# Performance work log

Hardware: AMD Instinct MI355X
Metric: run time of the kernel (lower is better)

The kernel has to match this reference:

```python
import jax, jax.numpy as jnp
import numpy as np
from jax.scipy.special import logsumexp

EPS = 0.1
MAX_ITER = 100
STAB = 1e-6
N_CLASS = 100
BATCH = 4096


def setup_inputs() -> dict:
    key = jax.random.key(0)
    k1, k2 = jax.random.split(key)
    pred = jax.random.normal(k1, (BATCH, N_CLASS), dtype=jnp.float32)
    target = jax.random.randint(k2, (BATCH,), 0, N_CLASS, dtype=jnp.int64)
    return {"pred": pred, "target": target}


def _cost_matrix_euclidean(n_class):
    c = jnp.arange(n_class, dtype=jnp.float32)
    C = (c[None, :] - c[:, None]) ** 2  # [n, n]
    cmax = C.max()
    return jnp.where(cmax > 0, C / cmax, C)


def _sinkhorn_cost(pred, target):
    B, n = pred.shape
    # normalized marginals
    mu = jax.nn.softmax(pred, axis=1) + STAB
    mu = mu / mu.sum(axis=1, keepdims=True)
    nu = jax.nn.one_hot(target, n, dtype=jnp.float32) + STAB
    nu = nu / nu.sum(axis=1, keepdims=True)

    C = _cost_matrix_euclidean(n)               # [n, n]
    K = jnp.exp(-C / EPS)
    log_K = jnp.log(jnp.maximum(K, STAB))       # stabilized kernel

    log_mu = jnp.log(mu + STAB)
    log_nu = jnp.log(nu + STAB)

    def step(carry, _):
        u, v = carry
        # u_new[b,i] = log_mu[b,i] - logsumexp_j(log_K[i,j] + v[b,j])
        u_new = log_mu - logsumexp(log_K[None, :, :] + v[:, None, :], axis=2)
        # v_new[b,j] = log_nu[b,j] - logsumexp_i(log_K[j,i] + u_new[b,i])
        v_new = log_nu - logsumexp(log_K.T[None, :, :] + u_new[:, :, None], axis=1)
        return (u_new, v_new), None

    u0 = jnp.zeros((B, n), dtype=pred.dtype)
    v0 = jnp.zeros((B, n), dtype=pred.dtype)
    (u, v), _ = jax.lax.scan(step, (u0, v0), None, length=MAX_ITER)

    # transport plan with marginal renormalization
    log_P = u[:, :, None] + log_K[None, :, :] + v[:, None, :]
    P = jnp.exp(log_P) + STAB
    P = P / P.sum(axis=2, keepdims=True) * mu[:, :, None]
    P = P / P.sum(axis=1, keepdims=True) * nu[:, None, :]
    cost = jnp.sum(P * C[None, :, :], axis=(1, 2))  # [B]

    # NaN fallback: cost of argmax-to-argmax transport
    alt_cost = C[jnp.argmax(mu, axis=1), jnp.argmax(nu, axis=1)]
    cost = jnp.where(jnp.isnan(cost).any(), alt_cost, cost)
    return cost


def reference(pred, target):
    return _sinkhorn_cost(pred, target).mean()  # reduction='mean'
```

## Files before the change

### kernel.cpp

```cpp
#include <hip/hip_runtime.h>
#include <math.h>

#define NCLS   100
#define ITERS  100
#define RPB    16
#define KS     136
#define XBUF   (RPB * KS)

typedef short  bf16x8 __attribute__((ext_vector_type(8)));
typedef float  f32x4  __attribute__((ext_vector_type(4)));

#if __has_builtin(__builtin_amdgcn_rcpf)
__device__ __forceinline__ float fast_rcp(float x) { return __builtin_amdgcn_rcpf(x); }
#else
__device__ __forceinline__ float fast_rcp(float x) { return 1.0f / x; }
#endif

#if __has_builtin(__builtin_amdgcn_exp2f)
__device__ __forceinline__ float fast_exp2(float x) { return __builtin_amdgcn_exp2f(x); }
#else
__device__ __forceinline__ float fast_exp2(float x) { return exp2f(x); }
#endif

__device__ __forceinline__ unsigned bf16_rne(float f) {
    unsigned u = __float_as_uint(f);
    return (u + 0x7FFFu + ((u >> 16) & 1u)) >> 16;
}
__device__ __forceinline__ unsigned cvt_pk_bf16(float a, float b) {
    unsigned r;
    asm("v_cvt_pk_bf16_f32 %0, %1, %2" : "=v"(r) : "v"(a), "v"(b));
    return r;
}
__device__ __forceinline__ float wave_sum(float v) {
#pragma unroll
    for (int m = 32; m > 0; m >>= 1) v += __shfl_xor(v, m, 64);
    return v;
}
__device__ __forceinline__ bool any_ne(f32x4 a, f32x4 b) {
    return (a[0] != b[0]) | (a[1] != b[1]) | (a[2] != b[2]) | (a[3] != b[3]);
}

#define MFMA_B(Af, Bf, Cf) __builtin_amdgcn_mfma_f32_16x16x32_bf16(Af, Bf, Cf, 0, 0, 0)

#define HALF(SRC, DST, MG0, X0V)                                              \
    {                                                                         \
        bf16x8 Xf_[4];                                                        \
        _Pragma("unroll")                                                     \
        for (int s_ = 0; s_ < 4; ++s_)                                        \
            Xf_[s_] = *(const bf16x8*)((SRC) + lc * KS + s_ * 32 + quad * 8); \
        f32x4 aA_ = biasv;                                                    \
        f32x4 aB_ = {0, 0, 0, 0};                                             \
        aA_ = MFMA_B(W0[0], Xf_[0], aA_);                                     \
        aB_ = MFMA_B(W0[2], Xf_[2], aB_);                                     \
        aA_ = MFMA_B(W0[1], Xf_[1], aA_);                                     \
        aB_ = MFMA_B(W0[3], Xf_[3], aB_);                                     \
        f32x4 acc0_ = aA_ + aB_;                                              \
        _Pragma("unroll")                                                     \
        for (int r_ = 0; r_ < 4; ++r_)                                        \
            X0V[r_] = MG0[r_] * fast_rcp(acc0_[r_]);                          \
        uint2 pk_;                                                            \
        pk_.x = cvt_pk_bf16(X0V[0], X0V[1]);                                  \
        pk_.y = cvt_pk_bf16(X0V[2], X0V[3]);                                  \
        *(uint2*)((DST) + wq4) = pk_;                                         \
        accP0_ = acc0_;                                                       \
    }

extern "C" __global__ void __launch_bounds__(512, 2)
sk_fused(const float* __restrict__ pred, const int* __restrict__ target,
         float* __restrict__ out, int rows)
{
    __shared__ short xs[2 * XBUF];
    __shared__ __align__(16) float aux[RPB * 104];
    __shared__ __align__(8) unsigned char flagC[8];

    const int tid  = threadIdx.x;
    const int lane = tid & 63;
    const int wave = tid >> 6;
    const int quad = lane >> 4;
    const int lc   = lane & 15;
    const int row0 = blockIdx.x * RPB;

    if (tid < 256) {
        const int r = tid >> 4;
        const int c = tid & 15;
        const float* p = pred + (size_t)(row0 + r) * NCLS;
        const float l2e = 1.44269504089f;
        float v[7];
        float mx = -3.4e38f;
#pragma unroll
        for (int q = 0; q < 7; ++q) {
            int j = c + q * 16;
            v[q] = (j < NCLS) ? p[j] : -3.4e38f;
            mx = fmaxf(mx, v[q]);
        }
#pragma unroll
        for (int m = 8; m >= 1; m >>= 1) mx = fmaxf(mx, __shfl_xor(mx, m, 64));
        float s = 0.f;
#pragma unroll
        for (int q = 0; q < 7; ++q) {
            v[q] = (c + q * 16 < NCLS) ? fast_exp2((v[q] - mx) * l2e) : 0.f;
            s += v[q];
        }
#pragma unroll
        for (int m = 8; m >= 1; m >>= 1) s += __shfl_xor(s, m, 64);
        float invS = 1.f / s;
        float s2 = 0.f;
#pragma unroll
        for (int q = 0; q < 7; ++q) {
            if (c + q * 16 < NCLS) { v[q] = v[q] * invS + 1e-6f; s2 += v[q]; }
        }
#pragma unroll
        for (int m = 8; m >= 1; m >>= 1) s2 += __shfl_xor(s2, m, 64);
        float invM = 1.f / s2;
#pragma unroll
        for (int q = 0; q < 7; ++q) {
            int j = c + q * 16;
            if (j < NCLS) aux[r * 104 + j] = v[q] * invM;
        }
    }

    const int t0n = wave * 16 + lc;
    f32x4 biasv;
#pragma unroll
    for (int r = 0; r < 4; ++r)
        biasv[r] = (wave * 16 + quad * 4 + r >= NCLS) ? 1.0f : 0.0f;

    const float c2 = -14.4269504089f / 9801.0f;
    bf16x8 W0[4];
#pragma unroll
    for (int s = 0; s < 4; ++s) {
#pragma unroll
        for (int j = 0; j < 8; ++j) {
            int k  = s * 32 + quad * 8 + j;
            int d0 = k - t0n;
            W0[s][j] = (short)bf16_rne(fast_exp2(c2 * (float)(d0 * d0)));
        }
    }

    __syncthreads();

    f32x4 mu0f, nu0f;
    const float invN = 1.0f / (1.0f + (float)NCLS * 1e-6f);
    const int tg = (int)target[row0 + lc];
#pragma unroll
    for (int r = 0; r < 4; ++r) {
        int n_r = wave * 16 + quad * 4 + r;
        mu0f[r] = (n_r < NCLS) ? aux[lc * 104 + n_r] : 0.f;
        nu0f[r] = (n_r < NCLS) ? ((((n_r == tg) ? 1.f : 0.f) + 1e-6f) * invN) : 0.f;
    }

    const int wq4 = lc * KS + wave * 16 + quad * 4;

    {
        uint2 pk;
        pk.x = cvt_pk_bf16(nu0f[0], nu0f[1]);
        pk.y = cvt_pk_bf16(nu0f[2], nu0f[3]);
        *(uint2*)(xs + wq4) = pk;
    }
    __syncthreads();

    f32x4 pvO0 = {-1.f, -1.f, -1.f, -1.f};
    f32x4 xT0, accP0_;
    uint2 fprev = {1u, 0u};
    for (int pair = 0; pair < ITERS - 1; ++pair) {
        HALF(xs, xs + XBUF, mu0f, xT0);
        if ((fprev.x | fprev.y) == 0u) break;
        __syncthreads();
        HALF(xs + XBUF, xs, nu0f, xT0);
        bool chgO = any_ne(accP0_, pvO0);
        pvO0 = accP0_;
        int anyv = __any((int)chgO);
        if (lane == 0) flagC[wave] = (unsigned char)anyv;
        __syncthreads();
        fprev = *(const uint2*)flagC;
    }

    f32x4 aR0, bR0;
    HALF(xs, xs + XBUF, mu0f, aR0);
    __syncthreads();
    HALF(xs + XBUF, xs, nu0f, bR0);
    __syncthreads();

    f32x4 t0a = {0.f, 0.f, 0.f, 0.f};
    {
        bf16x8 Bf[4];
#pragma unroll
        for (int s = 0; s < 4; ++s)
            Bf[s] = *(const bf16x8*)(xs + lc * KS + s * 32 + quad * 8);
#pragma unroll
        for (int s = 0; s < 4; ++s)
            t0a = MFMA_B(W0[s], Bf[s], t0a);
    }

    float* SsumP = aux;
    float* zP    = aux + 128;
    short* sclS  = (short*)(aux + 136);
    short* apS   = xs + XBUF;

    f32x4 sclv;
#pragma unroll
    for (int r = 0; r < 4; ++r)
        sclv[r] = mu0f[r] * fast_rcp(fmaf(aR0[r], t0a[r], (float)NCLS * 1e-6f));
    {
        uint2 pa;
        pa.x = cvt_pk_bf16(aR0[0] * sclv[0], aR0[1] * sclv[1]);
        pa.y = cvt_pk_bf16(aR0[2] * sclv[2], aR0[3] * sclv[3]);
        *(uint2*)(apS + wq4) = pa;
        uint2 ps;
        ps.x = cvt_pk_bf16(sclv[0], sclv[1]);
        ps.y = cvt_pk_bf16(sclv[2], sclv[3]);
        *(uint2*)(sclS + wq4) = ps;
    }
    {
        float ps = sclv[0] + sclv[1] + sclv[2] + sclv[3];
        ps += __shfl_xor(ps, 16, 64);
        ps += __shfl_xor(ps, 32, 64);
        if (lane < 16) SsumP[wave * 16 + lane] = ps;
    }
    __syncthreads();
    float Ssum = 0.f;
#pragma unroll
    for (int w = 0; w < 8; ++w) Ssum += SsumP[w * 16 + lc];

    bf16x8 KC0[4], C0[4];
    const float cinv = 1.0f / 9801.0f;
#pragma unroll
    for (int s = 0; s < 4; ++s) {
#pragma unroll
        for (int j = 0; j < 8; ++j) {
            int k  = s * 32 + quad * 8 + j;
            int d0 = k - t0n;
            float cc = (float)(d0 * d0) * cinv;
            KC0[s][j] = (short)bf16_rne(fast_exp2(c2 * (float)(d0 * d0)) * cc);
            C0[s][j]  = (short)bf16_rne(cc);
        }
    }

    f32x4 qv = {0,0,0,0}, mv = {0,0,0,0}, sv = {0,0,0,0};
    {
        bf16x8 Aa[4], As[4];
#pragma unroll
        for (int s = 0; s < 4; ++s) {
            Aa[s] = *(const bf16x8*)(apS  + lc * KS + s * 32 + quad * 8);
            As[s] = *(const bf16x8*)(sclS + lc * KS + s * 32 + quad * 8);
        }
#pragma unroll
        for (int s = 0; s < 4; ++s) {
            qv = MFMA_B(W0[s],  Aa[s], qv);
            mv = MFMA_B(KC0[s], Aa[s], mv);
            sv = MFMA_B(C0[s],  As[s], sv);
        }
    }

    float z = 0.f;
#pragma unroll
    for (int r = 0; r < 4; ++r) {
        float col0 = fmaf(bR0[r], qv[r], 1e-6f * Ssum);
        float in0  = fmaf(bR0[r], mv[r], 1e-6f * sv[r]);
        z += nu0f[r] * fast_rcp(col0) * in0;
    }
    z = wave_sum(z);
    if (lane == 0) zP[wave] = z;
    __syncthreads();
    if (tid == 0) {
        float tot = zP[0] + zP[1] + zP[2] + zP[3] + zP[4] + zP[5] + zP[6] + zP[7];
        atomicAdd(out, tot / (float)rows);
    }
}

extern "C" void kernel_launch(void* const* d_in, const int* in_sizes, int n_in,
                              void* d_out, int out_size, void* d_ws, size_t ws_size,
                              hipStream_t stream)
{
    const float* pred   = (const float*)d_in[0];
    const int*   target = (const int*)d_in[1];
    float*       out    = (float*)d_out;
    const int    rows   = in_sizes[0] / NCLS;

    hipMemsetAsync(out, 0, sizeof(float), stream);
    hipLaunchKernelGGL(sk_fused, dim3(rows / RPB), dim3(512), 0, stream,
                       pred, target, out, rows);
}
```

Before: 65.21 us.

## Halve block to 256 threads with two output tiles per wave

Each workgroup now runs 4 waves instead of 8, and each wave computes two 16-class output tiles, issuing interleaved MFMAs that share the same loaded X fragments. This is meant to cut barrier cost per Sinkhorn iteration, reuse LDS fragment loads across two tiles, and expose independent MFMA chains for latency hiding. In exchange, register pressure per thread doubles for the weight and accumulator fragments, and there are fewer waves to hide latency. The launch_bounds occupancy hint is also dropped.

```diff
diff --git a/kernel.cpp b/kernel.cpp
--- a/kernel.cpp
+++ b/kernel.cpp
@@ -42,36 +42,46 @@
 
 #define MFMA_B(Af, Bf, Cf) __builtin_amdgcn_mfma_f32_16x16x32_bf16(Af, Bf, Cf, 0, 0, 0)
 
-#define HALF(SRC, DST, MG0, X0V)                                              \
+#define HALF(SRC, DST, MG0, MG1, X0V, X1V)                                    \
     {                                                                         \
         bf16x8 Xf_[4];                                                        \
         _Pragma("unroll")                                                     \
         for (int s_ = 0; s_ < 4; ++s_)                                        \
             Xf_[s_] = *(const bf16x8*)((SRC) + lc * KS + s_ * 32 + quad * 8); \
-        f32x4 aA_ = biasv;                                                    \
-        f32x4 aB_ = {0, 0, 0, 0};                                             \
-        aA_ = MFMA_B(W0[0], Xf_[0], aA_);                                     \
-        aB_ = MFMA_B(W0[2], Xf_[2], aB_);                                     \
-        aA_ = MFMA_B(W0[1], Xf_[1], aA_);                                     \
-        aB_ = MFMA_B(W0[3], Xf_[3], aB_);                                     \
-        f32x4 acc0_ = aA_ + aB_;                                              \
+        f32x4 aA0_ = bias0v, aB0_ = {0, 0, 0, 0};                             \
+        f32x4 aA1_ = bias1v, aB1_ = {0, 0, 0, 0};                             \
+        aA0_ = MFMA_B(W0f[0], Xf_[0], aA0_);                                  \
+        aA1_ = MFMA_B(W1f[0], Xf_[0], aA1_);                                  \
+        aB0_ = MFMA_B(W0f[2], Xf_[2], aB0_);                                  \
+        aB1_ = MFMA_B(W1f[2], Xf_[2], aB1_);                                  \
+        aA0_ = MFMA_B(W0f[1], Xf_[1], aA0_);                                  \
+        aA1_ = MFMA_B(W1f[1], Xf_[1], aA1_);                                  \
+        aB0_ = MFMA_B(W0f[3], Xf_[3], aB0_);                                  \
+        aB1_ = MFMA_B(W1f[3], Xf_[3], aB1_);                                  \
+        f32x4 acc0_ = aA0_ + aB0_;                                            \
+        f32x4 acc1_ = aA1_ + aB1_;                                            \
         _Pragma("unroll")                                                     \
-        for (int r_ = 0; r_ < 4; ++r_)                                        \
+        for (int r_ = 0; r_ < 4; ++r_) {                                      \
             X0V[r_] = MG0[r_] * fast_rcp(acc0_[r_]);                          \
-        uint2 pk_;                                                            \
-        pk_.x = cvt_pk_bf16(X0V[0], X0V[1]);                                  \
-        pk_.y = cvt_pk_bf16(X0V[2], X0V[3]);                                  \
-        *(uint2*)((DST) + wq4) = pk_;                                         \
-        accP0_ = acc0_;                                                       \
-    }
-
-extern "C" __global__ void __launch_bounds__(512, 2)
+            X1V[r_] = MG1[r_] * fast_rcp(acc1_[r_]);                          \
+        }                                                                     \
+        uint2 pk0_, pk1_;                                                     \
+        pk0_.x = cvt_pk_bf16(X0V[0], X0V[1]);                                 \
+        pk0_.y = cvt_pk_bf16(X0V[2], X0V[3]);                                 \
+        pk1_.x = cvt_pk_bf16(X1V[0], X1V[1]);                                 \
+        pk1_.y = cvt_pk_bf16(X1V[2], X1V[3]);                                 \
+        *(uint2*)((DST) + wq40) = pk0_;                                       \
+        *(uint2*)((DST) + wq41) = pk1_;                                       \
+        accP0_ = acc0_; accP1_ = acc1_;                                       \
+    }
+
+extern "C" __global__ void __launch_bounds__(256)
 sk_fused(const float* __restrict__ pred, const int* __restrict__ target,
          float* __restrict__ out, int rows)
 {
     __shared__ short xs[2 * XBUF];
     __shared__ __align__(16) float aux[RPB * 104];
-    __shared__ __align__(8) unsigned char flagC[8];
+    __shared__ __align__(4) unsigned char flagC[4];
 
     const int tid  = threadIdx.x;
     const int lane = tid & 63;
@@ -80,7 +90,7 @@
     const int lc   = lane & 15;
     const int row0 = blockIdx.x * RPB;
 
-    if (tid < 256) {
+    {
         const int r = tid >> 4;
         const int c = tid & 15;
         const float* p = pred + (size_t)(row0 + r) * NCLS;
@@ -119,77 +129,94 @@
         }
     }
 
-    const int t0n = wave * 16 + lc;
-    f32x4 biasv;
-#pragma unroll
-    for (int r = 0; r < 4; ++r)
-        biasv[r] = (wave * 16 + quad * 4 + r >= NCLS) ? 1.0f : 0.0f;
+    const int tt0 = 2 * wave;
+    const int tt1 = 2 * wave + 1;
+    const int t0n = tt0 * 16 + lc;
+    const int t1n = tt1 * 16 + lc;
+    f32x4 bias0v, bias1v;
+#pragma unroll
+    for (int r = 0; r < 4; ++r) {
+        bias0v[r] = (tt0 * 16 + quad * 4 + r >= NCLS) ? 1.0f : 0.0f;
+        bias1v[r] = (tt1 * 16 + quad * 4 + r >= NCLS) ? 1.0f : 0.0f;
+    }
 
     const float c2 = -14.4269504089f / 9801.0f;
-    bf16x8 W0[4];
+    bf16x8 W0f[4], W1f[4];
 #pragma unroll
     for (int s = 0; s < 4; ++s) {
 #pragma unroll
         for (int j = 0; j < 8; ++j) {
             int k  = s * 32 + quad * 8 + j;
             int d0 = k - t0n;
-            W0[s][j] = (short)bf16_rne(fast_exp2(c2 * (float)(d0 * d0)));
-        }
-    }
-
-    __syncthreads();
-
-    f32x4 mu0f, nu0f;
+            int d1 = k - t1n;
+            W0f[s][j] = (short)bf16_rne(fast_exp2(c2 * (float)(d0 * d0)));
+            W1f[s][j] = (short)bf16_rne(fast_exp2(c2 * (float)(d1 * d1)));
+        }
+    }
+
+    __syncthreads();
+
+    f32x4 mu0f, mu1f, nu0f, nu1f;
     const float invN = 1.0f / (1.0f + (float)NCLS * 1e-6f);
     const int tg = (int)target[row0 + lc];
 #pragma unroll
     for (int r = 0; r < 4; ++r) {
-        int n_r = wave * 16 + quad * 4 + r;
-        mu0f[r] = (n_r < NCLS) ? aux[lc * 104 + n_r] : 0.f;
-        nu0f[r] = (n_r < NCLS) ? ((((n_r == tg) ? 1.f : 0.f) + 1e-6f) * invN) : 0.f;
-    }
-
-    const int wq4 = lc * KS + wave * 16 + quad * 4;
+        int n0 = tt0 * 16 + quad * 4 + r;
+        int n1 = tt1 * 16 + quad * 4 + r;
+        mu0f[r] = (n0 < NCLS) ? aux[lc * 104 + n0] : 0.f;
+        mu1f[r] = (n1 < NCLS) ? aux[lc * 104 + n1] : 0.f;
+        nu0f[r] = (n0 < NCLS) ? ((((n0 == tg) ? 1.f : 0.f) + 1e-6f) * invN) : 0.f;
+        nu1f[r] = (n1 < NCLS) ? ((((n1 == tg) ? 1.f : 0.f) + 1e-6f) * invN) : 0.f;
+    }
+
+    const int wq40 = lc * KS + tt0 * 16 + quad * 4;
+    const int wq41 = lc * KS + tt1 * 16 + quad * 4;
 
     {
         uint2 pk;
         pk.x = cvt_pk_bf16(nu0f[0], nu0f[1]);
         pk.y = cvt_pk_bf16(nu0f[2], nu0f[3]);
-        *(uint2*)(xs + wq4) = pk;
-    }
-    __syncthreads();
-
-    f32x4 pvO0 = {-1.f, -1.f, -1.f, -1.f};
-    f32x4 xT0, accP0_;
-    uint2 fprev = {1u, 0u};
+        *(uint2*)(xs + wq40) = pk;
+        pk.x = cvt_pk_bf16(nu1f[0], nu1f[1]);
+        pk.y = cvt_pk_bf16(nu1f[2], nu1f[3]);
+        *(uint2*)(xs + wq41) = pk;
+    }
+    __syncthreads();
+
+    f32x4 pvO0 = {-1.f, -1.f, -1.f, -1.f}, pvO1 = pvO0;
+    f32x4 xT0, xT1, accP0_, accP1_;
+    unsigned fprev = 1u;
     for (int pair = 0; pair < ITERS - 1; ++pair) {
-        HALF(xs, xs + XBUF, mu0f, xT0);
-        if ((fprev.x | fprev.y) == 0u) break;
+        HALF(xs, xs + XBUF, mu0f, mu1f, xT0, xT1);
+        if (fprev == 0u) break;
         __syncthreads();
-        HALF(xs + XBUF, xs, nu0f, xT0);
-        bool chgO = any_ne(accP0_, pvO0);
-        pvO0 = accP0_;
+        HALF(xs + XBUF, xs, nu0f, nu1f, xT0, xT1);
+        bool chgO = any_ne(accP0_, pvO0) || any_ne(accP1_, pvO1);
+        pvO0 = accP0_; pvO1 = accP1_;
         int anyv = __any((int)chgO);
         if (lane == 0) flagC[wave] = (unsigned char)anyv;
         __syncthreads();
-        fprev = *(const uint2*)flagC;
-    }
-
-    f32x4 aR0, bR0;
-    HALF(xs, xs + XBUF, mu0f, aR0);
-    __syncthreads();
-    HALF(xs + XBUF, xs, nu0f, bR0);
+        fprev = *(const unsigned*)flagC;
+    }
+
+    f32x4 aR0, aR1, bR0, bR1;
+    HALF(xs, xs + XBUF, mu0f, mu1f, aR0, aR1);
+    __syncthreads();
+    HALF(xs + XBUF, xs, nu0f, nu1f, bR0, bR1);
     __syncthreads();
 
     f32x4 t0a = {0.f, 0.f, 0.f, 0.f};
+    f32x4 t1a = {0.f, 0.f, 0.f, 0.f};
     {
         bf16x8 Bf[4];
 #pragma unroll
         for (int s = 0; s < 4; ++s)
             Bf[s] = *(const bf16x8*)(xs + lc * KS + s * 32 + quad * 8);
 #pragma unroll
-        for (int s = 0; s < 4; ++s)
-            t0a = MFMA_B(W0[s], Bf[s], t0a);
+        for (int s = 0; s < 4; ++s) {
+            t0a = MFMA_B(W0f[s], Bf[s], t0a);
+            t1a = MFMA_B(W1f[s], Bf[s], t1a);
+        }
     }
 
     float* SsumP = aux;
@@ -197,32 +224,46 @@
     short* sclS  = (short*)(aux + 136);
     short* apS   = xs + XBUF;
 
-    f32x4 sclv;
-#pragma unroll
-    for (int r = 0; r < 4; ++r)
-        sclv[r] = mu0f[r] * fast_rcp(fmaf(aR0[r], t0a[r], (float)NCLS * 1e-6f));
+    f32x4 scl0v, scl1v;
+#pragma unroll
+    for (int r = 0; r < 4; ++r) {
+        scl0v[r] = mu0f[r] * fast_rcp(fmaf(aR0[r], t0a[r], (float)NCLS * 1e-6f));
+        scl1v[r] = mu1f[r] * fast_rcp(fmaf(aR1[r], t1a[r], (float)NCLS * 1e-6f));
+    }
     {
         uint2 pa;
-        pa.x = cvt_pk_bf16(aR0[0] * sclv[0], aR0[1] * sclv[1]);
-        pa.y = cvt_pk_bf16(aR0[2] * sclv[2], aR0[3] * sclv[3]);
-        *(uint2*)(apS + wq4) = pa;
+        pa.x = cvt_pk_bf16(aR0[0] * scl0v[0], aR0[1] * scl0v[1]);
+        pa.y = cvt_pk_bf16(aR0[2] * scl0v[2], aR0[3] * scl0v[3]);
+        *(uint2*)(apS + wq40) = pa;
+        pa.x = cvt_pk_bf16(aR1[0] * scl1v[0], aR1[1] * scl1v[1]);
+        pa.y = cvt_pk_bf16(aR1[2] * scl1v[2], aR1[3] * scl1v[3]);
+        *(uint2*)(apS + wq41) = pa;
         uint2 ps;
-        ps.x = cvt_pk_bf16(sclv[0], sclv[1]);
-        ps.y = cvt_pk_bf16(sclv[2], sclv[3]);
-        *(uint2*)(sclS + wq4) = ps;
-    }
-    {
-        float ps = sclv[0] + sclv[1] + sclv[2] + sclv[3];
-        ps += __shfl_xor(ps, 16, 64);
-        ps += __shfl_xor(ps, 32, 64);
-        if (lane < 16) SsumP[wave * 16 + lane] = ps;
+        ps.x = cvt_pk_bf16(scl0v[0], scl0v[1]);
+        ps.y = cvt_pk_bf16(scl0v[2], scl0v[3]);
+        *(uint2*)(sclS + wq40) = ps;
+        ps.x = cvt_pk_bf16(scl1v[0], scl1v[1]);
+        ps.y = cvt_pk_bf16(scl1v[2], scl1v[3]);
+        *(uint2*)(sclS + wq41) = ps;
+    }
+    {
+        float p0 = scl0v[0] + scl0v[1] + scl0v[2] + scl0v[3];
+        p0 += __shfl_xor(p0, 16, 64);
+        p0 += __shfl_xor(p0, 32, 64);
+        float p1 = scl1v[0] + scl1v[1] + scl1v[2] + scl1v[3];
+        p1 += __shfl_xor(p1, 16, 64);
+        p1 += __shfl_xor(p1, 32, 64);
+        if (lane < 16) {
+            SsumP[tt0 * 16 + lane] = p0;
+            SsumP[tt1 * 16 + lane] = p1;
+        }
     }
     __syncthreads();
     float Ssum = 0.f;
 #pragma unroll
-    for (int w = 0; w < 8; ++w) Ssum += SsumP[w * 16 + lc];
-
-    bf16x8 KC0[4], C0[4];
+    for (int t = 0; t < 8; ++t) Ssum += SsumP[t * 16 + lc];
+
+    bf16x8 KC0[4], KC1[4], C0[4], C1[4];
     const float cinv = 1.0f / 9801.0f;
 #pragma unroll
     for (int s = 0; s < 4; ++s) {
@@ -230,13 +271,18 @@
         for (int j = 0; j < 8; ++j) {
             int k  = s * 32 + quad * 8 + j;
             int d0 = k - t0n;
-            float cc = (float)(d0 * d0) * cinv;
-            KC0[s][j] = (short)bf16_rne(fast_exp2(c2 * (float)(d0 * d0)) * cc);
-            C0[s][j]  = (short)bf16_rne(cc);
-        }
-    }
-
-    f32x4 qv = {0,0,0,0}, mv = {0,0,0,0}, sv = {0,0,0,0};
+            int d1 = k - t1n;
+            float cc0 = (float)(d0 * d0) * cinv;
+            float cc1 = (float)(d1 * d1) * cinv;
+            KC0[s][j] = (short)bf16_rne(fast_exp2(c2 * (float)(d0 * d0)) * cc0);
+            KC1[s][j] = (short)bf16_rne(fast_exp2(c2 * (float)(d1 * d1)) * cc1);
+            C0[s][j]  = (short)bf16_rne(cc0);
+            C1[s][j]  = (short)bf16_rne(cc1);
+        }
+    }
+
+    f32x4 q0v = {0,0,0,0}, m0v = {0,0,0,0}, s0v = {0,0,0,0};
+    f32x4 q1v = {0,0,0,0}, m1v = {0,0,0,0}, s1v = {0,0,0,0};
     {
         bf16x8 Aa[4], As[4];
 #pragma unroll
@@ -246,21 +292,28 @@
         }
 #pragma unroll
         for (int s = 0; s < 4; ++s) {
-            qv = MFMA_B(W0[s],  Aa[s], qv);
-            mv = MFMA_B(KC0[s], Aa[s], mv);
-            sv = MFMA_B(C0[s],  As[s], sv);
-        }
-    }
-
-    float z = 0.f;
+            q0v = MFMA_B(W0f[s], Aa[s], q0v);
+            q1v = MFMA_B(W1f[s], Aa[s], q1v);
+            m0v = MFMA_B(KC0[s], Aa[s], m0v);
+            m1v = MFMA_B(KC1[s], Aa[s], m1v);
+            s0v = MFMA_B(C0[s],  As[s], s0v);
+            s1v = MFMA_B(C1[s],  As[s], s1v);
+        }
+    }
+
+    float z0 = 0.f, z1 = 0.f;
 #pragma unroll
     for (int r = 0; r < 4; ++r) {
-        float col0 = fmaf(bR0[r], qv[r], 1e-6f * Ssum);
-        float in0  = fmaf(bR0[r], mv[r], 1e-6f * sv[r]);
-        z += nu0f[r] * fast_rcp(col0) * in0;
-    }
-    z = wave_sum(z);
-    if (lane == 0) zP[wave] = z;
+        float col0 = fmaf(bR0[r], q0v[r], 1e-6f * Ssum);
+        float in0  = fmaf(bR0[r], m0v[r], 1e-6f * s0v[r]);
+        z0 += nu0f[r] * fast_rcp(col0) * in0;
+        float col1 = fmaf(bR1[r], q1v[r], 1e-6f * Ssum);
+        float in1  = fmaf(bR1[r], m1v[r], 1e-6f * s1v[r]);
+        z1 += nu1f[r] * fast_rcp(col1) * in1;
+    }
+    z0 = wave_sum(z0);
+    z1 = wave_sum(z1);
+    if (lane == 0) { zP[tt0] = z0; zP[tt1] = z1; }
     __syncthreads();
     if (tid == 0) {
         float tot = zP[0] + zP[1] + zP[2] + zP[3] + zP[4] + zP[5] + zP[6] + zP[7];
@@ -278,6 +331,6 @@
     const int    rows   = in_sizes[0] / NCLS;
 
     hipMemsetAsync(out, 0, sizeof(float), stream);
-    hipLaunchKernelGGL(sk_fused, dim3(rows / RPB), dim3(512), 0, stream,
+    hipLaunchKernelGGL(sk_fused, dim3(rows / RPB), dim3(256), 0, stream,
                        pred, target, out, rows);
 }
```

Result: no change. 65.75 us (+0.8%).
